# Kernel tuning notes

Hardware: AMD Instinct MI355X
Metric: run time of the kernel (lower is better)

Reference implementation:

```python
import jax, jax.numpy as jnp
import numpy as np

IN_F, OUT_F, GROUP = 4096, 11008, 128
TOKENS = 64


def setup_inputs() -> dict:
    key = jax.random.key(0)
    k1, k2, k3, k4 = jax.random.split(key, 4)
    x = jax.random.normal(k1, (TOKENS, IN_F), dtype=jnp.float32).astype(jnp.float16)
    # packed uint8 values stored in int32 (two int4 nibbles per byte)
    w_packed = jax.random.randint(k2, (IN_F, OUT_F // 2), 0, 256, dtype=jnp.int32)
    num_groups = IN_F // GROUP
    w_scale = (jax.random.uniform(k3, (num_groups, OUT_F), minval=1e-3, maxval=0.1)).astype(jnp.float16)
    w_zero = jnp.round(jax.random.uniform(k4, (num_groups, OUT_F), minval=0.0, maxval=15.0)).astype(jnp.float16)
    return {"x": x, "w_packed": w_packed, "w_scale": w_scale, "w_zero": w_zero}


def _dequantize_int4(w_packed, w_scale, w_zero, group_size=GROUP):
    in_f = w_packed.shape[0]
    out_f = w_packed.shape[1] * 2
    w_low = (w_packed & 15).astype(jnp.float16)          # even output columns
    w_high = ((w_packed >> 4) & 15).astype(jnp.float16)  # odd output columns
    # interleave low/high -> [in_f, out_f]
    w_int4 = jnp.stack([w_low, w_high], axis=-1).reshape(in_f, out_f)
    num_groups = in_f // group_size
    w_g = w_int4.reshape(num_groups, group_size, out_f)
    w = (w_g - w_zero[:, None, :]) * w_scale[:, None, :]
    return w.reshape(in_f, out_f)


def reference(x, w_packed, w_scale, w_zero):
    w = _dequantize_int4(w_packed, w_scale, w_zero)  # [in_f, out_f] fp16
    return jnp.matmul(x.astype(jnp.float16), w)      # [tokens, out_f]
```

## Files before the change

### kernel.cpp

```cpp
#include <hip/hip_runtime.h>
#include <stdint.h>

#define IN_F   4096
#define OUT_F  11008
#define C32    5504
#define LDST   72
#define KHALF  2048
#define NST    32

typedef __attribute__((ext_vector_type(8))) _Float16 half8;
typedef __attribute__((ext_vector_type(4))) float floatx4;

static __device__ __forceinline__ uint32_t pkh(float a, float b) {
    auto h = __builtin_amdgcn_cvt_pkrtz(a, b);
    union { decltype(h) v; uint32_t u; } r; r.v = h; return r.u;
}

__global__ __launch_bounds__(256) void prep_kernel(
    const float* __restrict__ x, uint32_t* __restrict__ xh, float4* __restrict__ out4)
{
    int tid = blockIdx.x * 256 + threadIdx.x;
    if (tid < (64 * OUT_F / 4)) out4[tid] = make_float4(0.f, 0.f, 0.f, 0.f);
    if (tid < (64 * IN_F / 2)) {
        float2 v = ((const float2*)x)[tid];
        xh[tid] = pkh(v.x, v.y);
    }
}

__global__ __launch_bounds__(256, 4) void int4_gemm_kernel(
    const int*      __restrict__ wp,
    const float*    __restrict__ wscale,
    const float*    __restrict__ wzero,
    const uint32_t* __restrict__ xh,
    float*          __restrict__ out)
{
    __shared__ float4 tab[16 * 16];
    __shared__ __align__(16) ushort bld[2][32 * LDST];

    const int tid   = threadIdx.x;
    const int col0  = blockIdx.x * 32;
    const int ky    = blockIdx.y;
    const int kbase = ky * KHALF;

    const int c  = tid & 15;
    const int kb = (tid >> 4) * 4;
    const int ce = 2 * c, co = ce + 1;
    const int* wbase = wp + (size_t)(kbase + kb) * C32 + (col0 >> 1) + c;

    const int wave = tid >> 6;
    const int lane = tid & 63;
    const int g    = lane >> 4;
    const int bc0  = lane & 15;
    const int bc1  = bc0 + 16;
    const uint32_t* xbase = xh + (size_t)(wave * 16 + bc0) * (IN_F / 2) + (kbase >> 1) + g * 4;

    {
        int gg = tid >> 4, cp = tid & 15;
        size_t b = (size_t)(ky * 16 + gg) * OUT_F + col0 + 2 * cp;
        float se = wscale[b], so = wscale[b + 1];
        float ze = wzero[b],  zo = wzero[b + 1];
        tab[tid] = make_float4(se, ze * se, so, zo * so);
    }

    floatx4 acc0 = {0.f, 0.f, 0.f, 0.f}, acc1 = {0.f, 0.f, 0.f, 0.f};

    struct Pref { uint32_t q0, q1, q2, q3; };
    auto issue = [&](int st) {
        const int* p = wbase + (size_t)st * (64 * (size_t)C32);
        Pref P;
        P.q0 = (uint32_t)p[0];
        P.q1 = (uint32_t)p[C32];
        P.q2 = (uint32_t)p[2 * C32];
        P.q3 = (uint32_t)p[3 * C32];
        return P;
    };

    auto dq_write = [&](ushort* buf, const Pref& P, int st) {
        float4 t = tab[((st >> 1) << 4) + c];
        float l0 = fmaf((float)( P.q0        & 15u), t.x, -t.y);
        float l1 = fmaf((float)( P.q1        & 15u), t.x, -t.y);
        float l2 = fmaf((float)( P.q2        & 15u), t.x, -t.y);
        float l3 = fmaf((float)( P.q3        & 15u), t.x, -t.y);
        float h0 = fmaf((float)((P.q0 >> 4)  & 15u), t.z, -t.w);
        float h1 = fmaf((float)((P.q1 >> 4)  & 15u), t.z, -t.w);
        float h2 = fmaf((float)((P.q2 >> 4)  & 15u), t.z, -t.w);
        float h3 = fmaf((float)((P.q3 >> 4)  & 15u), t.z, -t.w);
        *(uint2*)(buf + ce * LDST + kb) = make_uint2(pkh(l0, l1), pkh(l2, l3));
        *(uint2*)(buf + co * LDST + kb) = make_uint2(pkh(h0, h1), pkh(h2, h3));
    };

    auto compute = [&](const ushort* buf, int st) {
        union { uint4 u; half8 h; } a0, a1;
        a0.u = *(const uint4*)(xbase + (size_t)st * 32);
        a1.u = *(const uint4*)(xbase + (size_t)st * 32 + 16);
        half8 B00 = *(const half8*)(buf + bc0 * LDST + g * 8);
        half8 B01 = *(const half8*)(buf + bc0 * LDST + 32 + g * 8);
        half8 B10 = *(const half8*)(buf + bc1 * LDST + g * 8);
        half8 B11 = *(const half8*)(buf + bc1 * LDST + 32 + g * 8);
        acc0 = __builtin_amdgcn_mfma_f32_16x16x32_f16(a0.h, B00, acc0, 0, 0, 0);
        acc1 = __builtin_amdgcn_mfma_f32_16x16x32_f16(a0.h, B10, acc1, 0, 0, 0);
        acc0 = __builtin_amdgcn_mfma_f32_16x16x32_f16(a1.h, B01, acc0, 0, 0, 0);
        acc1 = __builtin_amdgcn_mfma_f32_16x16x32_f16(a1.h, B11, acc1, 0, 0, 0);
    };

    Pref P = issue(0);
    __syncthreads();
    dq_write(bld[0], P, 0);
    P = issue(1);
    asm volatile("s_waitcnt lgkmcnt(0)");
    __builtin_amdgcn_s_barrier();

    #pragma unroll 2
    for (int st = 0; st < NST; ++st) {
        if (st + 1 < NST) {
            Pref Pn = (st + 2 < NST) ? issue(st + 2) : P;
            dq_write(bld[(st + 1) & 1], P, st + 1);
            P = Pn;
        }
        compute(bld[st & 1], st);
        asm volatile("s_waitcnt lgkmcnt(0)");
        __builtin_amdgcn_s_barrier();
    }

    const int ocol = col0 + bc0;
    const int rb   = wave * 16 + g * 4;
    #pragma unroll
    for (int r = 0; r < 4; ++r) {
        unsafeAtomicAdd(out + (size_t)(rb + r) * OUT_F + ocol,      acc0[r]);
        unsafeAtomicAdd(out + (size_t)(rb + r) * OUT_F + ocol + 16, acc1[r]);
    }
}

extern "C" void kernel_launch(void* const* d_in, const int* in_sizes, int n_in,
                              void* d_out, int out_size, void* d_ws, size_t ws_size,
                              hipStream_t stream) {
    const float* x      = (const float*)d_in[0];
    const int*   wp     = (const int*)  d_in[1];
    const float* wscale = (const float*)d_in[2];
    const float* wzero  = (const float*)d_in[3];
    float*       out    = (float*)d_out;
    uint32_t*    xh     = (uint32_t*)d_ws;
    (void)in_sizes; (void)n_in; (void)out_size; (void)ws_size;

    prep_kernel<<<dim3(688), dim3(256), 0, stream>>>(x, xh, (float4*)out);
    int4_gemm_kernel<<<dim3(344, 2), dim3(256), 0, stream>>>(wp, wscale, wzero, xh, out);
}
```

Before: 41.44 us.

## Split K four ways, deepen weight prefetch, swizzle LDS, and prefetch activations

The K split goes from 2 to 4 blocks per column tile, doubling grid parallelism (344x4 blocks). Weight loads are now nontemporal and prefetched three stages ahead in a rotating register buffer. Activation fragments are loaded one stage ahead. The padded LDS layout is replaced with an XOR-style swizzle. The cost is more atomic adds to the output and higher register pressure from the deeper prefetch.

New measurement: 57.56 us. 1.39x slower.

```diff
diff --git a/kernel.cpp b/kernel.cpp
--- a/kernel.cpp
+++ b/kernel.cpp
@@ -4,9 +4,10 @@
 #define IN_F   4096
 #define OUT_F  11008
 #define C32    5504
-#define LDST   72
-#define KHALF  2048
-#define NST    32
+#define KSPL   4
+#define KBLK   1024
+#define NST    16
+#define NGRP   8
 
 typedef __attribute__((ext_vector_type(8))) _Float16 half8;
 typedef __attribute__((ext_vector_type(4))) float floatx4;
@@ -34,13 +35,13 @@
     const uint32_t* __restrict__ xh,
     float*          __restrict__ out)
 {
-    __shared__ float4 tab[16 * 16];
-    __shared__ __align__(16) ushort bld[2][32 * LDST];
+    __shared__ float4 tab[NGRP * 16];
+    __shared__ __align__(16) ushort bld[2][32 * 64];
 
     const int tid   = threadIdx.x;
     const int col0  = blockIdx.x * 32;
     const int ky    = blockIdx.y;
-    const int kbase = ky * KHALF;
+    const int kbase = ky * KBLK;
 
     const int c  = tid & 15;
     const int kb = (tid >> 4) * 4;
@@ -54,9 +55,19 @@
     const int bc1  = bc0 + 16;
     const uint32_t* xbase = xh + (size_t)(wave * 16 + bc0) * (IN_F / 2) + (kbase >> 1) + g * 4;
 
-    {
+    auto baddr = [](int col, int k) {
+        return col * 128 + ((((k >> 3) + col) & 7) << 4) + ((k & 7) << 1);
+    };
+    const int we  = baddr(ce,  kb);
+    const int wo  = baddr(co,  kb);
+    const int r00 = baddr(bc0, g * 8);
+    const int r01 = baddr(bc0, 32 + g * 8);
+    const int r10 = baddr(bc1, g * 8);
+    const int r11 = baddr(bc1, 32 + g * 8);
+
+    if (tid < NGRP * 16) {
         int gg = tid >> 4, cp = tid & 15;
-        size_t b = (size_t)(ky * 16 + gg) * OUT_F + col0 + 2 * cp;
+        size_t b = (size_t)(ky * NGRP + gg) * OUT_F + col0 + 2 * cp;
         float se = wscale[b], so = wscale[b + 1];
         float ze = wzero[b],  zo = wzero[b + 1];
         tab[tid] = make_float4(se, ze * se, so, zo * so);
@@ -68,10 +79,10 @@
     auto issue = [&](int st) {
         const int* p = wbase + (size_t)st * (64 * (size_t)C32);
         Pref P;
-        P.q0 = (uint32_t)p[0];
-        P.q1 = (uint32_t)p[C32];
-        P.q2 = (uint32_t)p[2 * C32];
-        P.q3 = (uint32_t)p[3 * C32];
+        P.q0 = (uint32_t)__builtin_nontemporal_load(p);
+        P.q1 = (uint32_t)__builtin_nontemporal_load(p + C32);
+        P.q2 = (uint32_t)__builtin_nontemporal_load(p + 2 * C32);
+        P.q3 = (uint32_t)__builtin_nontemporal_load(p + 3 * C32);
         return P;
     };
 
@@ -85,39 +96,45 @@
         float h1 = fmaf((float)((P.q1 >> 4)  & 15u), t.z, -t.w);
         float h2 = fmaf((float)((P.q2 >> 4)  & 15u), t.z, -t.w);
         float h3 = fmaf((float)((P.q3 >> 4)  & 15u), t.z, -t.w);
-        *(uint2*)(buf + ce * LDST + kb) = make_uint2(pkh(l0, l1), pkh(l2, l3));
-        *(uint2*)(buf + co * LDST + kb) = make_uint2(pkh(h0, h1), pkh(h2, h3));
+        *(uint2*)((char*)buf + we) = make_uint2(pkh(l0, l1), pkh(l2, l3));
+        *(uint2*)((char*)buf + wo) = make_uint2(pkh(h0, h1), pkh(h2, h3));
     };
 
-    auto compute = [&](const ushort* buf, int st) {
-        union { uint4 u; half8 h; } a0, a1;
-        a0.u = *(const uint4*)(xbase + (size_t)st * 32);
-        a1.u = *(const uint4*)(xbase + (size_t)st * 32 + 16);
-        half8 B00 = *(const half8*)(buf + bc0 * LDST + g * 8);
-        half8 B01 = *(const half8*)(buf + bc0 * LDST + 32 + g * 8);
-        half8 B10 = *(const half8*)(buf + bc1 * LDST + g * 8);
-        half8 B11 = *(const half8*)(buf + bc1 * LDST + 32 + g * 8);
-        acc0 = __builtin_amdgcn_mfma_f32_16x16x32_f16(a0.h, B00, acc0, 0, 0, 0);
-        acc1 = __builtin_amdgcn_mfma_f32_16x16x32_f16(a0.h, B10, acc1, 0, 0, 0);
-        acc0 = __builtin_amdgcn_mfma_f32_16x16x32_f16(a1.h, B01, acc0, 0, 0, 0);
-        acc1 = __builtin_amdgcn_mfma_f32_16x16x32_f16(a1.h, B11, acc1, 0, 0, 0);
-    };
-
-    Pref P = issue(0);
+    Pref Ps[3];
+    Ps[0] = issue(0); Ps[1] = issue(1); Ps[2] = issue(2);
+    uint4 A0 = *(const uint4*)(xbase);
+    uint4 A1 = *(const uint4*)(xbase + 16);
     __syncthreads();
-    dq_write(bld[0], P, 0);
-    P = issue(1);
+    dq_write(bld[0], Ps[0], 0);
+    Ps[0] = issue(3);
     asm volatile("s_waitcnt lgkmcnt(0)");
     __builtin_amdgcn_s_barrier();
 
-    #pragma unroll 2
+    #pragma unroll
     for (int st = 0; st < NST; ++st) {
+        const char* bb = (const char*)bld[st & 1];
+        half8 B00 = *(const half8*)(bb + r00);
+        half8 B01 = *(const half8*)(bb + r01);
+        half8 B10 = *(const half8*)(bb + r10);
+        half8 B11 = *(const half8*)(bb + r11);
+
+        if (st + 1 < NST) dq_write(bld[(st + 1) & 1], Ps[(st + 1) % 3], st + 1);
+        if (st + 4 < NST) Ps[(st + 1) % 3] = issue(st + 4);
+
+        uint4 An0 = A0, An1 = A1;
         if (st + 1 < NST) {
-            Pref Pn = (st + 2 < NST) ? issue(st + 2) : P;
-            dq_write(bld[(st + 1) & 1], P, st + 1);
-            P = Pn;
+            An0 = *(const uint4*)(xbase + (st + 1) * 32);
+            An1 = *(const uint4*)(xbase + (st + 1) * 32 + 16);
         }
-        compute(bld[st & 1], st);
+
+        union { uint4 u; half8 h; } ua0, ua1;
+        ua0.u = A0; ua1.u = A1;
+        acc0 = __builtin_amdgcn_mfma_f32_16x16x32_f16(ua0.h, B00, acc0, 0, 0, 0);
+        acc1 = __builtin_amdgcn_mfma_f32_16x16x32_f16(ua0.h, B10, acc1, 0, 0, 0);
+        acc0 = __builtin_amdgcn_mfma_f32_16x16x32_f16(ua1.h, B01, acc0, 0, 0, 0);
+        acc1 = __builtin_amdgcn_mfma_f32_16x16x32_f16(ua1.h, B11, acc1, 0, 0, 0);
+        A0 = An0; A1 = An1;
+
         asm volatile("s_waitcnt lgkmcnt(0)");
         __builtin_amdgcn_s_barrier();
     }
@@ -143,5 +160,5 @@
     (void)in_sizes; (void)n_in; (void)out_size; (void)ws_size;
 
     prep_kernel<<<dim3(688), dim3(256), 0, stream>>>(x, xh, (float4*)out);
-    int4_gemm_kernel<<<dim3(344, 2), dim3(256), 0, stream>>>(wp, wscale, wzero, xh, out);
+    int4_gemm_kernel<<<dim3(344, KSPL), dim3(256), 0, stream>>>(wp, wscale, wzero, xh, out);
 }
```

## Deepen weight prefetch to four stages and prefetch activations one step ahead

Applied to the files above, without the earlier changes.

The packed-weight prefetch queue grows from one stage ahead to four stages ahead, using a rotating register array, so more global loads are in flight per thread. Activation fragments for the next k-step are also loaded one iteration early so their latency is hidden behind the MFMAs. This raises register use, which may lower occupancy under the 4-blocks-per-CU launch bound, in exchange for better latency hiding in this memory-bound loop.

Result: slower. 44.73 us (+8.0%).

```diff
diff --git a/kernel.cpp b/kernel.cpp
--- a/kernel.cpp
+++ b/kernel.cpp
@@ -89,35 +89,42 @@
         *(uint2*)(buf + co * LDST + kb) = make_uint2(pkh(h0, h1), pkh(h2, h3));
     };
 
-    auto compute = [&](const ushort* buf, int st) {
-        union { uint4 u; half8 h; } a0, a1;
-        a0.u = *(const uint4*)(xbase + (size_t)st * 32);
-        a1.u = *(const uint4*)(xbase + (size_t)st * 32 + 16);
+    Pref P0 = issue(0);
+    Pref Ps[4];
+    Ps[1] = issue(1); Ps[2] = issue(2); Ps[3] = issue(3); Ps[0] = issue(4);
+    uint4 A0 = *(const uint4*)(xbase);
+    uint4 A1 = *(const uint4*)(xbase + 16);
+    __syncthreads();
+    dq_write(bld[0], P0, 0);
+    asm volatile("s_waitcnt lgkmcnt(0)");
+    __builtin_amdgcn_s_barrier();
+
+    #pragma unroll 4
+    for (int st = 0; st < NST; ++st) {
+        if (st + 1 < NST) {
+            dq_write(bld[(st + 1) & 1], Ps[(st + 1) & 3], st + 1);
+            if (st + 5 < NST) Ps[(st + 1) & 3] = issue(st + 5);
+        }
+
+        uint4 An0 = A0, An1 = A1;
+        if (st + 1 < NST) {
+            An0 = *(const uint4*)(xbase + (st + 1) * 32);
+            An1 = *(const uint4*)(xbase + (st + 1) * 32 + 16);
+        }
+
+        const ushort* buf = bld[st & 1];
         half8 B00 = *(const half8*)(buf + bc0 * LDST + g * 8);
         half8 B01 = *(const half8*)(buf + bc0 * LDST + 32 + g * 8);
         half8 B10 = *(const half8*)(buf + bc1 * LDST + g * 8);
         half8 B11 = *(const half8*)(buf + bc1 * LDST + 32 + g * 8);
-        acc0 = __builtin_amdgcn_mfma_f32_16x16x32_f16(a0.h, B00, acc0, 0, 0, 0);
-        acc1 = __builtin_amdgcn_mfma_f32_16x16x32_f16(a0.h, B10, acc1, 0, 0, 0);
-        acc0 = __builtin_amdgcn_mfma_f32_16x16x32_f16(a1.h, B01, acc0, 0, 0, 0);
-        acc1 = __builtin_amdgcn_mfma_f32_16x16x32_f16(a1.h, B11, acc1, 0, 0, 0);
-    };
+        union { uint4 u; half8 h; } ua0, ua1;
+        ua0.u = A0; ua1.u = A1;
+        acc0 = __builtin_amdgcn_mfma_f32_16x16x32_f16(ua0.h, B00, acc0, 0, 0, 0);
+        acc1 = __builtin_amdgcn_mfma_f32_16x16x32_f16(ua0.h, B10, acc1, 0, 0, 0);
+        acc0 = __builtin_amdgcn_mfma_f32_16x16x32_f16(ua1.h, B01, acc0, 0, 0, 0);
+        acc1 = __builtin_amdgcn_mfma_f32_16x16x32_f16(ua1.h, B11, acc1, 0, 0, 0);
+        A0 = An0; A1 = An1;
 
-    Pref P = issue(0);
-    __syncthreads();
-    dq_write(bld[0], P, 0);
-    P = issue(1);
-    asm volatile("s_waitcnt lgkmcnt(0)");
-    __builtin_amdgcn_s_barrier();
-
-    #pragma unroll 2
-    for (int st = 0; st < NST; ++st) {
-        if (st + 1 < NST) {
-            Pref Pn = (st + 2 < NST) ? issue(st + 2) : P;
-            dq_write(bld[(st + 1) & 1], P, st + 1);
-            P = Pn;
-        }
-        compute(bld[st & 1], st);
         asm volatile("s_waitcnt lgkmcnt(0)");
         __builtin_amdgcn_s_barrier();
     }
```

## Make each wave own a private 16-column B tile and drop block barriers

Applied to the files above, without the earlier changes.

Each wave now dequantizes its own 16 output columns into a private LDS double buffer and runs MFMAs for all four 16-row token tiles. This removes the block-wide barriers from the main loop. The K dimension is split four ways instead of two and blocks cover 64 columns, which raises the block count and the number of atomic adds to the output. Each wave rereads all of the activations from global/L2 and holds four accumulators, so register pressure and activation traffic go up. There is no explicit wait or barrier between an LDS write and the same wave's read, so correctness depends on the compiler inserting waitcnts.

After: 64.34 us. +55.3%, slower.

```diff
diff --git a/kernel.cpp b/kernel.cpp
--- a/kernel.cpp
+++ b/kernel.cpp
@@ -4,9 +4,11 @@
 #define IN_F   4096
 #define OUT_F  11008
 #define C32    5504
+#define KSPL   4
+#define KBLK   1024
+#define NST    16
+#define NGRP   8
 #define LDST   72
-#define KHALF  2048
-#define NST    32
 
 typedef __attribute__((ext_vector_type(8))) _Float16 half8;
 typedef __attribute__((ext_vector_type(4))) float floatx4;
@@ -34,100 +36,99 @@
     const uint32_t* __restrict__ xh,
     float*          __restrict__ out)
 {
-    __shared__ float4 tab[16 * 16];
-    __shared__ __align__(16) ushort bld[2][32 * LDST];
+    __shared__ float4 tab[NGRP * 32];
+    __shared__ __align__(16) ushort bld[4][2][16 * LDST];
 
     const int tid   = threadIdx.x;
-    const int col0  = blockIdx.x * 32;
-    const int ky    = blockIdx.y;
-    const int kbase = ky * KHALF;
+    const int wv    = tid >> 6;
+    const int l     = tid & 63;
+    const int col0  = blockIdx.x * 64;
+    const int wcol  = col0 + wv * 16;
+    const int kbase = blockIdx.y * KBLK;
 
-    const int c  = tid & 15;
-    const int kb = (tid >> 4) * 4;
-    const int ce = 2 * c, co = ce + 1;
-    const int* wbase = wp + (size_t)(kbase + kb) * C32 + (col0 >> 1) + c;
+    const int c = l & 7;
+    const int r = l >> 3;
+    const int* wbase = wp + (size_t)(kbase + r * 8) * C32 + (wcol >> 1) + c;
 
-    const int wave = tid >> 6;
-    const int lane = tid & 63;
-    const int g    = lane >> 4;
-    const int bc0  = lane & 15;
-    const int bc1  = bc0 + 16;
-    const uint32_t* xbase = xh + (size_t)(wave * 16 + bc0) * (IN_F / 2) + (kbase >> 1) + g * 4;
+    const int g  = l >> 4;
+    const int bc = l & 15;
+    const uint32_t* xbase = xh + (size_t)bc * (IN_F / 2) + (kbase >> 1) + g * 4;
 
     {
-        int gg = tid >> 4, cp = tid & 15;
-        size_t b = (size_t)(ky * 16 + gg) * OUT_F + col0 + 2 * cp;
+        int gg = tid >> 5, cp = tid & 31;
+        size_t b = (size_t)(blockIdx.y * NGRP + gg) * OUT_F + col0 + 2 * cp;
         float se = wscale[b], so = wscale[b + 1];
         float ze = wzero[b],  zo = wzero[b + 1];
         tab[tid] = make_float4(se, ze * se, so, zo * so);
     }
+    __syncthreads();
 
-    floatx4 acc0 = {0.f, 0.f, 0.f, 0.f}, acc1 = {0.f, 0.f, 0.f, 0.f};
+    ushort* buf0 = bld[wv][0];
+    ushort* buf1 = bld[wv][1];
 
-    struct Pref { uint32_t q0, q1, q2, q3; };
-    auto issue = [&](int st) {
+    floatx4 acc[4] = {{0.f,0.f,0.f,0.f},{0.f,0.f,0.f,0.f},
+                      {0.f,0.f,0.f,0.f},{0.f,0.f,0.f,0.f}};
+
+    auto load8 = [&](uint32_t* w, int st) {
         const int* p = wbase + (size_t)st * (64 * (size_t)C32);
-        Pref P;
-        P.q0 = (uint32_t)p[0];
-        P.q1 = (uint32_t)p[C32];
-        P.q2 = (uint32_t)p[2 * C32];
-        P.q3 = (uint32_t)p[3 * C32];
-        return P;
+        #pragma unroll
+        for (int j = 0; j < 8; ++j) w[j] = (uint32_t)p[j * C32];
     };
 
-    auto dq_write = [&](ushort* buf, const Pref& P, int st) {
-        float4 t = tab[((st >> 1) << 4) + c];
-        float l0 = fmaf((float)( P.q0        & 15u), t.x, -t.y);
-        float l1 = fmaf((float)( P.q1        & 15u), t.x, -t.y);
-        float l2 = fmaf((float)( P.q2        & 15u), t.x, -t.y);
-        float l3 = fmaf((float)( P.q3        & 15u), t.x, -t.y);
-        float h0 = fmaf((float)((P.q0 >> 4)  & 15u), t.z, -t.w);
-        float h1 = fmaf((float)((P.q1 >> 4)  & 15u), t.z, -t.w);
-        float h2 = fmaf((float)((P.q2 >> 4)  & 15u), t.z, -t.w);
-        float h3 = fmaf((float)((P.q3 >> 4)  & 15u), t.z, -t.w);
-        *(uint2*)(buf + ce * LDST + kb) = make_uint2(pkh(l0, l1), pkh(l2, l3));
-        *(uint2*)(buf + co * LDST + kb) = make_uint2(pkh(h0, h1), pkh(h2, h3));
+    auto dq_write = [&](ushort* buf, const uint32_t* w, int st) {
+        float4 t = tab[((st >> 1) << 5) + wv * 8 + c];
+        uint32_t lo[4], hi[4];
+        #pragma unroll
+        for (int j = 0; j < 4; ++j) {
+            float l0 = fmaf((float)( w[2*j]        & 15u), t.x, -t.y);
+            float l1 = fmaf((float)( w[2*j+1]      & 15u), t.x, -t.y);
+            float h0 = fmaf((float)((w[2*j]   >> 4) & 15u), t.z, -t.w);
+            float h1 = fmaf((float)((w[2*j+1] >> 4) & 15u), t.z, -t.w);
+            lo[j] = pkh(l0, l1);
+            hi[j] = pkh(h0, h1);
+        }
+        *(uint4*)(buf + (2*c)     * LDST + r*8) = *(uint4*)lo;
+        *(uint4*)(buf + (2*c + 1) * LDST + r*8) = *(uint4*)hi;
     };
 
     auto compute = [&](const ushort* buf, int st) {
-        union { uint4 u; half8 h; } a0, a1;
-        a0.u = *(const uint4*)(xbase + (size_t)st * 32);
-        a1.u = *(const uint4*)(xbase + (size_t)st * 32 + 16);
-        half8 B00 = *(const half8*)(buf + bc0 * LDST + g * 8);
-        half8 B01 = *(const half8*)(buf + bc0 * LDST + 32 + g * 8);
-        half8 B10 = *(const half8*)(buf + bc1 * LDST + g * 8);
-        half8 B11 = *(const half8*)(buf + bc1 * LDST + 32 + g * 8);
-        acc0 = __builtin_amdgcn_mfma_f32_16x16x32_f16(a0.h, B00, acc0, 0, 0, 0);
-        acc1 = __builtin_amdgcn_mfma_f32_16x16x32_f16(a0.h, B10, acc1, 0, 0, 0);
-        acc0 = __builtin_amdgcn_mfma_f32_16x16x32_f16(a1.h, B01, acc0, 0, 0, 0);
-        acc1 = __builtin_amdgcn_mfma_f32_16x16x32_f16(a1.h, B11, acc1, 0, 0, 0);
+        half8 B0 = *(const half8*)(buf + bc * LDST + g * 8);
+        half8 B1 = *(const half8*)(buf + bc * LDST + 32 + g * 8);
+        #pragma unroll
+        for (int rt = 0; rt < 4; ++rt) {
+            union { uint4 u; half8 h; } a0, a1;
+            a0.u = *(const uint4*)(xbase + (size_t)rt * 32768 + st * 32);
+            a1.u = *(const uint4*)(xbase + (size_t)rt * 32768 + st * 32 + 16);
+            acc[rt] = __builtin_amdgcn_mfma_f32_16x16x32_f16(a0.h, B0, acc[rt], 0, 0, 0);
+            acc[rt] = __builtin_amdgcn_mfma_f32_16x16x32_f16(a1.h, B1, acc[rt], 0, 0, 0);
+        }
     };
 
-    Pref P = issue(0);
-    __syncthreads();
-    dq_write(bld[0], P, 0);
-    P = issue(1);
-    asm volatile("s_waitcnt lgkmcnt(0)");
-    __builtin_amdgcn_s_barrier();
+    uint32_t wa[8], wb[8];
+    load8(wa, 0);
+    load8(wb, 1);
+    dq_write(buf0, wa, 0);
+    load8(wa, 2);
 
-    #pragma unroll 2
-    for (int st = 0; st < NST; ++st) {
-        if (st + 1 < NST) {
-            Pref Pn = (st + 2 < NST) ? issue(st + 2) : P;
-            dq_write(bld[(st + 1) & 1], P, st + 1);
-            P = Pn;
+    #pragma unroll 1
+    for (int st = 0; st < NST; st += 2) {
+        compute(buf0, st);
+        dq_write(buf1, wb, st + 1);
+        if (st + 3 < NST) load8(wb, st + 3);
+        compute(buf1, st + 1);
+        if (st + 2 < NST) {
+            dq_write(buf0, wa, st + 2);
+            if (st + 4 < NST) load8(wa, st + 4);
         }
-        compute(bld[st & 1], st);
-        asm volatile("s_waitcnt lgkmcnt(0)");
-        __builtin_amdgcn_s_barrier();
     }
 
-    const int ocol = col0 + bc0;
-    const int rb   = wave * 16 + g * 4;
+    const int ocol = wcol + bc;
     #pragma unroll
-    for (int r = 0; r < 4; ++r) {
-        unsafeAtomicAdd(out + (size_t)(rb + r) * OUT_F + ocol,      acc0[r]);
-        unsafeAtomicAdd(out + (size_t)(rb + r) * OUT_F + ocol + 16, acc1[r]);
+    for (int rt = 0; rt < 4; ++rt) {
+        #pragma unroll
+        for (int j = 0; j < 4; ++j) {
+            unsafeAtomicAdd(out + (size_t)(rt * 16 + g * 4 + j) * OUT_F + ocol, acc[rt][j]);
+        }
     }
 }
 
@@ -143,5 +144,5 @@
     (void)in_sizes; (void)n_in; (void)out_size; (void)ws_size;
 
     prep_kernel<<<dim3(688), dim3(256), 0, stream>>>(x, xh, (float4*)out);
-    int4_gemm_kernel<<<dim3(344, 2), dim3(256), 0, stream>>>(wp, wscale, wzero, xh, out);
+    int4_gemm_kernel<<<dim3(OUT_F / 64, KSPL), dim3(256), 0, stream>>>(wp, wscale, wzero, xh, out);
 }
```
